# Kernel optimization log

Measured on AMD Instinct MI355X. Metric: run time of the kernel, lower is better.

## Reference

```python
import jax, jax.numpy as jnp
import numpy as np

N = 131072
MUL = 128                      # multiplicity of each irrep block in the input
IN_DIM = MUL * (1 + 3 + 5)     # 128x0e + 128x1o + 128x2e = 1152
INV_SQRT_MUL = 1.0 / np.sqrt(MUL)  # e3nn o3.Linear path normalization (fan_in = 128)

# --- Clebsch-Gordan (wigner 3j) tensors for 1o x 1o -> 0e, 1e, 2e ------------
# e3nn real basis ordering for l=1 is (y, z, x): index 0=y, 1=z, 2=x.

def _w3j_110():
    # 0e output: dot product; sum of squares of entries = 1
    return np.eye(3, dtype=np.float32) / np.sqrt(3.0)

def _w3j_111():
    # 1e output: Levi-Civita (cross product), normalized so sum of squares = 1
    eps = np.zeros((3, 3, 3), np.float32)
    for i, j, k in [(0, 1, 2), (1, 2, 0), (2, 0, 1)]:
        eps[i, j, k] = 1.0
        eps[j, i, k] = -1.0
    return eps / np.sqrt(6.0)

def _w3j_112():
    # 2e output: symmetric traceless rank-2 part.
    # l=2 component order: (xy, yz, 3z^2-r^2, xz, x^2-y^2); l=1 axes (y,z,x).
    Y, Z, X = 0, 1, 2
    s2 = 1.0 / np.sqrt(2.0)
    s6 = 1.0 / np.sqrt(6.0)
    M = np.zeros((3, 3, 5), np.float32)
    M[X, Y, 0] = M[Y, X, 0] = s2
    M[Y, Z, 1] = M[Z, Y, 1] = s2
    M[X, X, 2] = -s6; M[Y, Y, 2] = -s6; M[Z, Z, 2] = 2.0 * s6
    M[X, Z, 3] = M[Z, X, 3] = s2
    M[X, X, 4] = s2; M[Y, Y, 4] = -s2
    return M / np.sqrt(5.0)

_C0 = jnp.asarray(_w3j_110())
_C1 = jnp.asarray(_w3j_111())
_C2 = jnp.asarray(_w3j_112())
# path weights sqrt(dim(irrep_out)) for irrep_normalization='component',
# path_normalization='element' with fan = mul1*mul2 = 1
_PW0 = 1.0
_PW1 = float(np.sqrt(3.0))
_PW2 = float(np.sqrt(5.0))


def setup_inputs() -> dict:
    key = jax.random.key(0)
    k1, k2, k3, k4 = jax.random.split(key, 4)
    x = jax.random.normal(k1, (N, IN_DIM), jnp.float32)
    W1 = jax.random.normal(k2, (MUL, MUL), jnp.float32)   # 128x1o -> 128x1o
    W2 = jax.random.normal(k3, (MUL, 2), jnp.float32)     # 128x1o -> 2x1o
    tp_w = jax.random.normal(k4, (3,), jnp.float32)       # one weight per CG path
    return {"x": x, "W1": W1, "W2": W2, "tp_w": tp_w}


def reference(x, W1, W2, tp_w):
    n = x.shape[0]
    # o3.Linear(128x0e+128x1o+128x2e -> 128x1o): only the 1o block connects.
    x1o = x[:, MUL:MUL + 3 * MUL].reshape(n, MUL, 3)
    y = jnp.einsum('nuc,uv->nvc', x1o, W1) * INV_SQRT_MUL   # [N,128,3]
    y = jax.nn.silu(y)                                      # elementwise, as in torch
    y = jnp.einsum('nuc,uv->nvc', y, W2) * INV_SQRT_MUL     # [N,2,3] == 2x1o
    a, b = y[:, 0], y[:, 1]                                 # split y[:, :3], y[:, 3:]
    out0 = (tp_w[0] * _PW0) * jnp.einsum('ij,ni,nj->n', _C0, a, b)[:, None]  # [N,1]
    out1 = (tp_w[1] * _PW1) * jnp.einsum('ijk,ni,nj->nk', _C1, a, b)          # [N,3]
    out2 = (tp_w[2] * _PW2) * jnp.einsum('ijk,ni,nj->nk', _C2, a, b)          # [N,5]
    return jnp.concatenate([out0, out1, out2], axis=-1)     # [N,9] (0e+1e+2e)
```

## Files before the change

### kernel.cpp

```cpp
#include <hip/hip_runtime.h>
#include <hip/hip_bf16.h>

#define MULC 128
#define IN_DIM 1152
#define ROWS_PER_WG 64
#define NTHREADS 256
#define W1T_PITCH 136

typedef __attribute__((ext_vector_type(8))) short bf16x8;
typedef __attribute__((ext_vector_type(4))) float f32x4;
typedef __attribute__((ext_vector_type(4))) unsigned short u16x4;

__device__ __forceinline__ unsigned short f2bf(float f) {
    unsigned int b = __builtin_bit_cast(unsigned int, f);
    b += 0x7fffu + ((b >> 16) & 1u);
    return (unsigned short)(b >> 16);
}

#define LOADC(r0,r1,r2,r3,r4,r5, kc) {                                  \
    const float4* p_ = (const float4*)(xbase + 96 * (kc));              \
    r0 = p_[0]; r1 = p_[1]; r2 = p_[2]; r3 = p_[3]; r4 = p_[4]; r5 = p_[5]; }

#define FRAGS(F0,F1,F2, r0,r1,r2,r3,r4,r5)                                         \
    bf16x8 F0 = { (short)f2bf(r0.x), (short)f2bf(r0.w), (short)f2bf(r1.z),         \
                  (short)f2bf(r2.y), (short)f2bf(r3.x), (short)f2bf(r3.w),         \
                  (short)f2bf(r4.z), (short)f2bf(r5.y) };                          \
    bf16x8 F1 = { (short)f2bf(r0.y), (short)f2bf(r1.x), (short)f2bf(r1.w),         \
                  (short)f2bf(r2.z), (short)f2bf(r3.y), (short)f2bf(r4.x),         \
                  (short)f2bf(r4.w), (short)f2bf(r5.z) };                          \
    bf16x8 F2 = { (short)f2bf(r0.z), (short)f2bf(r1.y), (short)f2bf(r2.x),         \
                  (short)f2bf(r2.w), (short)f2bf(r3.z), (short)f2bf(r4.y),         \
                  (short)f2bf(r5.x), (short)f2bf(r5.w) };

#define MFMA_STEP(kc, F0,F1,F2)                                                     \
    _Pragma("unroll")                                                               \
    for (int nt = 0; nt < 8; ++nt) {                                                \
        bf16x8 bfr = *(const bf16x8*)&lds[(nt * 16 + li) * W1T_PITCH + (kc) * 32 + g * 8]; \
        acc[0][nt] = __builtin_amdgcn_mfma_f32_16x16x32_bf16(F0, bfr, acc[0][nt], 0, 0, 0); \
        acc[1][nt] = __builtin_amdgcn_mfma_f32_16x16x32_bf16(F1, bfr, acc[1][nt], 0, 0, 0); \
        acc[2][nt] = __builtin_amdgcn_mfma_f32_16x16x32_bf16(F2, bfr, acc[2][nt], 0, 0, 0); \
    }

__global__ __launch_bounds__(NTHREADS, 2)
void nltp_kernel(const float* __restrict__ x, const float* __restrict__ W1,
                 const float* __restrict__ W2, const float* __restrict__ tpw,
                 float* __restrict__ out)
{
    __shared__ __align__(16) unsigned short lds[128 * W1T_PITCH];
    const int t  = threadIdx.x;
    const int n0 = blockIdx.x * ROWS_PER_WG;
    const int l  = t & 63;
    const int w  = t >> 6;
    const int g  = l >> 4;
    const int li = l & 15;

    const float* xbase = x + (size_t)(n0 + 16 * w + li) * IN_DIM + MULC + 24 * g;

    float4 a0,a1,a2,a3,a4,a5, b0,b1,b2,b3,b4,b5;
    LOADC(a0,a1,a2,a3,a4,a5, 0);

    for (int it = 0; it < 16; ++it) {
        int tau = it * 256 + t;
        int v   = tau & 127;
        int u   = (tau >> 7) * 4;
        float f0 = W1[(u + 0) * MULC + v];
        float f1 = W1[(u + 1) * MULC + v];
        float f2 = W1[(u + 2) * MULC + v];
        float f3 = W1[(u + 3) * MULC + v];
        u16x4 pk = { f2bf(f0), f2bf(f1), f2bf(f2), f2bf(f3) };
        *(u16x4*)&lds[v * W1T_PITCH + u] = pk;
    }
    __syncthreads();

    f32x4 acc[3][8];
#pragma unroll
    for (int c = 0; c < 3; ++c)
#pragma unroll
        for (int nt = 0; nt < 8; ++nt)
            acc[c][nt] = (f32x4){0.f, 0.f, 0.f, 0.f};

    LOADC(b0,b1,b2,b3,b4,b5, 1);
    { FRAGS(fa0,fa1,fa2, a0,a1,a2,a3,a4,a5); MFMA_STEP(0, fa0,fa1,fa2); }
    LOADC(a0,a1,a2,a3,a4,a5, 2);
    { FRAGS(fb0,fb1,fb2, b0,b1,b2,b3,b4,b5); MFMA_STEP(1, fb0,fb1,fb2); }
    LOADC(b0,b1,b2,b3,b4,b5, 3);
    { FRAGS(fc0,fc1,fc2, a0,a1,a2,a3,a4,a5); MFMA_STEP(2, fc0,fc1,fc2); }
    { FRAGS(fd0,fd1,fd2, b0,b1,b2,b3,b4,b5); MFMA_STEP(3, fd0,fd1,fd2); }

    const float inv = 0.08838834764831845f;
    float w2a[8], w2b[8];
#pragma unroll
    for (int nt = 0; nt < 8; ++nt) {
        float2 p = *(const float2*)(W2 + 2 * (nt * 16 + li));
        w2a[nt] = p.x; w2b[nt] = p.y;
    }
    float pa[3][4], pb[3][4];
#pragma unroll
    for (int c = 0; c < 3; ++c)
#pragma unroll
        for (int rg = 0; rg < 4; ++rg) { pa[c][rg] = 0.f; pb[c][rg] = 0.f; }

#pragma unroll
    for (int c = 0; c < 3; ++c)
#pragma unroll
        for (int nt = 0; nt < 8; ++nt)
#pragma unroll
            for (int rg = 0; rg < 4; ++rg) {
                float y = acc[c][nt][rg] * inv;
                float s = y / (1.f + __expf(-y));
                pa[c][rg] += s * w2a[nt];
                pb[c][rg] += s * w2b[nt];
            }

#pragma unroll
    for (int c = 0; c < 3; ++c)
#pragma unroll
        for (int rg = 0; rg < 4; ++rg) {
            float va = pa[c][rg], vb = pb[c][rg];
            va += __shfl_xor(va, 1, 16); vb += __shfl_xor(vb, 1, 16);
            va += __shfl_xor(va, 2, 16); vb += __shfl_xor(vb, 2, 16);
            va += __shfl_xor(va, 4, 16); vb += __shfl_xor(vb, 4, 16);
            va += __shfl_xor(va, 8, 16); vb += __shfl_xor(vb, 8, 16);
            pa[c][rg] = va * inv;
            pb[c][rg] = vb * inv;
        }

    const float tw0 = tpw[0], tw1 = tpw[1], tw2 = tpw[2];
    const float k0 = tw0 * 0.5773502691896258f;
    const float k1 = tw1 * 0.7071067811865476f;
    const float s2 = 0.7071067811865476f;
    const float s6 = 0.4082482904638631f;

#pragma unroll
    for (int rg = 0; rg < 4; ++rg) {
        float a_0 = pa[0][rg], a_1 = pa[1][rg], a_2 = pa[2][rg];
        float b_0 = pb[0][rg], b_1 = pb[1][rg], b_2 = pb[2][rg];
        float o0 = k0 * (a_0 * b_0 + a_1 * b_1 + a_2 * b_2);
        float o1 = k1 * (a_1 * b_2 - a_2 * b_1);
        float o2 = k1 * (a_2 * b_0 - a_0 * b_2);
        float o3 = k1 * (a_0 * b_1 - a_1 * b_0);
        float o4 = tw2 * (s2 * (a_2 * b_0 + a_0 * b_2));
        float o5 = tw2 * (s2 * (a_0 * b_1 + a_1 * b_0));
        float o6 = tw2 * (s6 * (2.f * a_1 * b_1 - a_2 * b_2 - a_0 * b_0));
        float o7 = tw2 * (s2 * (a_2 * b_1 + a_1 * b_2));
        float o8 = tw2 * (s2 * (a_2 * b_2 - a_0 * b_0));
        float o = li == 0 ? o0 : li == 1 ? o1 : li == 2 ? o2 : li == 3 ? o3 :
                  li == 4 ? o4 : li == 5 ? o5 : li == 6 ? o6 : li == 7 ? o7 : o8;
        if (li < 9) {
            int row = n0 + 16 * w + 4 * g + rg;
            out[row * 9 + li] = o;
        }
    }
}

extern "C" void kernel_launch(void* const* d_in, const int* in_sizes, int n_in,
                              void* d_out, int out_size, void* d_ws, size_t ws_size,
                              hipStream_t stream) {
    const float* x   = (const float*)d_in[0];
    const float* W1  = (const float*)d_in[1];
    const float* W2  = (const float*)d_in[2];
    const float* tpw = (const float*)d_in[3];
    float* out = (float*)d_out;
    const int n = in_sizes[0] / IN_DIM;
    dim3 grid(n / ROWS_PER_WG);
    nltp_kernel<<<grid, NTHREADS, 0, stream>>>(x, W1, W2, tpw, out);
}
```

Baseline: 64.73 us.

## Use nontemporal loads, deeper prefetch, hardware bf16 convert and rcp in SiLU

Loads of x now use nontemporal loads, and two chunks are prefetched before the W1 staging loop so that global latency overlaps the LDS fill. The extra register set adds one more stage of load pipelining. The manual bf16 rounding is replaced with the __float2bfloat16 intrinsic, and the SiLU division is replaced with a hardware reciprocal. The risks are higher register pressure from the third fragment buffer, and a slight accuracy change from the approximate reciprocal.

```diff
diff --git a/kernel.cpp b/kernel.cpp
--- a/kernel.cpp
+++ b/kernel.cpp
@@ -3,7 +3,6 @@
 
 #define MULC 128
 #define IN_DIM 1152
-#define ROWS_PER_WG 64
 #define NTHREADS 256
 #define W1T_PITCH 136
 
@@ -11,30 +10,28 @@
 typedef __attribute__((ext_vector_type(4))) float f32x4;
 typedef __attribute__((ext_vector_type(4))) unsigned short u16x4;
 
-__device__ __forceinline__ unsigned short f2bf(float f) {
-    unsigned int b = __builtin_bit_cast(unsigned int, f);
-    b += 0x7fffu + ((b >> 16) & 1u);
-    return (unsigned short)(b >> 16);
+__device__ __forceinline__ short bfu(float f) {
+    __hip_bfloat16 h = __float2bfloat16(f);
+    return __builtin_bit_cast(short, h);
 }
 
-#define LOADC(r0,r1,r2,r3,r4,r5, kc) {                                  \
-    const float4* p_ = (const float4*)(xbase + 96 * (kc));              \
-    r0 = p_[0]; r1 = p_[1]; r2 = p_[2]; r3 = p_[3]; r4 = p_[4]; r5 = p_[5]; }
+#define LOADC(R, kc) {                                                   \
+    const f32x4* p_ = (const f32x4*)(xbase + 96 * (kc));                 \
+    _Pragma("unroll")                                                    \
+    for (int m_ = 0; m_ < 6; ++m_) R[m_] = __builtin_nontemporal_load(p_ + m_); }
 
-#define FRAGS(F0,F1,F2, r0,r1,r2,r3,r4,r5)                                         \
-    bf16x8 F0 = { (short)f2bf(r0.x), (short)f2bf(r0.w), (short)f2bf(r1.z),         \
-                  (short)f2bf(r2.y), (short)f2bf(r3.x), (short)f2bf(r3.w),         \
-                  (short)f2bf(r4.z), (short)f2bf(r5.y) };                          \
-    bf16x8 F1 = { (short)f2bf(r0.y), (short)f2bf(r1.x), (short)f2bf(r1.w),         \
-                  (short)f2bf(r2.z), (short)f2bf(r3.y), (short)f2bf(r4.x),         \
-                  (short)f2bf(r4.w), (short)f2bf(r5.z) };                          \
-    bf16x8 F2 = { (short)f2bf(r0.z), (short)f2bf(r1.y), (short)f2bf(r2.x),         \
-                  (short)f2bf(r2.w), (short)f2bf(r3.z), (short)f2bf(r4.y),         \
-                  (short)f2bf(r5.x), (short)f2bf(r5.w) };
+#define FRAGS(F0, F1, F2, R)                                             \
+    bf16x8 F0, F1, F2;                                                   \
+    _Pragma("unroll")                                                    \
+    for (int s_ = 0; s_ < 8; ++s_) {                                     \
+        F0[s_] = bfu(R[(3 * s_ + 0) >> 2][(3 * s_ + 0) & 3]);            \
+        F1[s_] = bfu(R[(3 * s_ + 1) >> 2][(3 * s_ + 1) & 3]);            \
+        F2[s_] = bfu(R[(3 * s_ + 2) >> 2][(3 * s_ + 2) & 3]);            \
+    }
 
-#define MFMA_STEP(kc, F0,F1,F2)                                                     \
-    _Pragma("unroll")                                                               \
-    for (int nt = 0; nt < 8; ++nt) {                                                \
+#define MFMA_STEP(kc, F0, F1, F2)                                        \
+    _Pragma("unroll")                                                    \
+    for (int nt = 0; nt < 8; ++nt) {                                     \
         bf16x8 bfr = *(const bf16x8*)&lds[(nt * 16 + li) * W1T_PITCH + (kc) * 32 + g * 8]; \
         acc[0][nt] = __builtin_amdgcn_mfma_f32_16x16x32_bf16(F0, bfr, acc[0][nt], 0, 0, 0); \
         acc[1][nt] = __builtin_amdgcn_mfma_f32_16x16x32_bf16(F1, bfr, acc[1][nt], 0, 0, 0); \
@@ -48,7 +45,7 @@
 {
     __shared__ __align__(16) unsigned short lds[128 * W1T_PITCH];
     const int t  = threadIdx.x;
-    const int n0 = blockIdx.x * ROWS_PER_WG;
+    const int n0 = blockIdx.x * 64;
     const int l  = t & 63;
     const int w  = t >> 6;
     const int g  = l >> 4;
@@ -56,8 +53,9 @@
 
     const float* xbase = x + (size_t)(n0 + 16 * w + li) * IN_DIM + MULC + 24 * g;
 
-    float4 a0,a1,a2,a3,a4,a5, b0,b1,b2,b3,b4,b5;
-    LOADC(a0,a1,a2,a3,a4,a5, 0);
+    f32x4 A[6], B[6], C[6];
+    LOADC(A, 0);
+    LOADC(B, 1);
 
     for (int it = 0; it < 16; ++it) {
         int tau = it * 256 + t;
@@ -67,7 +65,8 @@
         float f1 = W1[(u + 1) * MULC + v];
         float f2 = W1[(u + 2) * MULC + v];
         float f3 = W1[(u + 3) * MULC + v];
-        u16x4 pk = { f2bf(f0), f2bf(f1), f2bf(f2), f2bf(f3) };
+        u16x4 pk = { (unsigned short)bfu(f0), (unsigned short)bfu(f1),
+                     (unsigned short)bfu(f2), (unsigned short)bfu(f3) };
         *(u16x4*)&lds[v * W1T_PITCH + u] = pk;
     }
     __syncthreads();
@@ -79,13 +78,12 @@
         for (int nt = 0; nt < 8; ++nt)
             acc[c][nt] = (f32x4){0.f, 0.f, 0.f, 0.f};
 
-    LOADC(b0,b1,b2,b3,b4,b5, 1);
-    { FRAGS(fa0,fa1,fa2, a0,a1,a2,a3,a4,a5); MFMA_STEP(0, fa0,fa1,fa2); }
-    LOADC(a0,a1,a2,a3,a4,a5, 2);
-    { FRAGS(fb0,fb1,fb2, b0,b1,b2,b3,b4,b5); MFMA_STEP(1, fb0,fb1,fb2); }
-    LOADC(b0,b1,b2,b3,b4,b5, 3);
-    { FRAGS(fc0,fc1,fc2, a0,a1,a2,a3,a4,a5); MFMA_STEP(2, fc0,fc1,fc2); }
-    { FRAGS(fd0,fd1,fd2, b0,b1,b2,b3,b4,b5); MFMA_STEP(3, fd0,fd1,fd2); }
+    LOADC(C, 2);
+    { FRAGS(fa0, fa1, fa2, A); MFMA_STEP(0, fa0, fa1, fa2); }
+    LOADC(A, 3);
+    { FRAGS(fb0, fb1, fb2, B); MFMA_STEP(1, fb0, fb1, fb2); }
+    { FRAGS(fc0, fc1, fc2, C); MFMA_STEP(2, fc0, fc1, fc2); }
+    { FRAGS(fd0, fd1, fd2, A); MFMA_STEP(3, fd0, fd1, fd2); }
 
     const float inv = 0.08838834764831845f;
     float w2a[8], w2b[8];
@@ -107,7 +105,8 @@
 #pragma unroll
             for (int rg = 0; rg < 4; ++rg) {
                 float y = acc[c][nt][rg] * inv;
-                float s = y / (1.f + __expf(-y));
+                float e = __expf(-y);
+                float s = y * __builtin_amdgcn_rcpf(1.f + e);
                 pa[c][rg] += s * w2a[nt];
                 pb[c][rg] += s * w2b[nt];
             }
@@ -162,6 +161,6 @@
     const float* tpw = (const float*)d_in[3];
     float* out = (float*)d_out;
     const int n = in_sizes[0] / IN_DIM;
-    dim3 grid(n / ROWS_PER_WG);
+    dim3 grid(n / 64);
     nltp_kernel<<<grid, NTHREADS, 0, stream>>>(x, W1, W2, tpw, out);
 }
```

After: 98.46 us. 1.52x slower.
